# Performance work log

Hardware: AMD Instinct MI355X
Metric: run time of the kernel (lower is better)

Reference implementation:

```python
import jax, jax.numpy as jnp
import numpy as np

B, L, D, H, S = 4, 4096, 1024, 16, 4
DH = D // H


def setup_inputs() -> dict:
    key = jax.random.key(0)
    ks = jax.random.split(key, 12)
    std = 0.02
    inp = {
        "x": jax.random.normal(ks[0], (B, L, D), jnp.float32),
        "scale_logits": jax.random.normal(ks[1], (S,), jnp.float32),
        "wq": jax.random.normal(ks[2], (D, D), jnp.float32) * std,
        "bq": jnp.zeros((D,), jnp.float32),
        "wk": jax.random.normal(ks[3], (D, D), jnp.float32) * std,
        "bk": jnp.zeros((D,), jnp.float32),
        "wv": jax.random.normal(ks[4], (D, D), jnp.float32) * std,
        "bv": jnp.zeros((D,), jnp.float32),
        "wo": jax.random.normal(ks[5], (D, D), jnp.float32) * std,
        "bo": jnp.zeros((D,), jnp.float32),
        "ws": jax.random.normal(ks[6], (S, D, D), jnp.float32) * std,  # per-scale Linear weights (out,in)
        "bs": jax.random.normal(ks[7], (S, D), jnp.float32) * std,
    }
    return inp


def reference(x, scale_logits, wq, bq, wk, bk, wv, bv, wo, bo, ws, bs):
    # q/k/v projections; kept flat (B,L,D) since the torch code re-flattens before scale proj
    qf = x @ wq.T + bq
    kf = x @ wk.T + bk
    vf = x @ wv.T + bv
    # per-scale linear projection, vectorized over scales: (B,S,L,D)
    sq = jnp.einsum('bld,sed->bsle', qf, ws) + bs[None, :, None, :]
    sk = jnp.einsum('bld,sed->bsle', kf, ws) + bs[None, :, None, :]
    sv = jnp.einsum('bld,sed->bsle', vf, ws) + bs[None, :, None, :]
    sq = sq.reshape(B, S, L, H, DH)
    sk = sk.reshape(B, S, L, H, DH)
    sv = sv.reshape(B, S, L, H, DH)
    # faithful to torch: matmul over last two dims of (B,L,H,dh) -> per-position
    # head-mixing scores of shape (B,S,L,H,H)
    scale = 1.0 / np.sqrt(DH).astype(np.float32)
    scores = jnp.einsum('bslhd,bslgd->bslhg', sq, sk) * scale
    attn = jax.nn.softmax(scores, axis=-1)
    out = jnp.einsum('bslhg,bslgd->bslhd', attn, sv)  # (B,S,L,H,DH)
    w = jax.nn.softmax(scale_logits, axis=0)  # (S,)
    combined = jnp.einsum('s,bslhd->blhd', w, out).reshape(B, L, D)
    return combined @ wo.T + bo
```

## Files before the change

### kernel.cpp

```cpp
#include <hip/hip_runtime.h>


typedef unsigned short u16;
typedef __attribute__((ext_vector_type(8))) short s16x8;
typedef __attribute__((ext_vector_type(8))) unsigned short u16x8;
typedef __attribute__((ext_vector_type(4))) float f32x4;

#define MM 16384
#define DDIM 1024
#define DDSQ 1048576ull

__device__ __forceinline__ u16 f2bf(float f) {
  unsigned u = __float_as_uint(f);
  u = (u + 0x7FFFu + ((u >> 16) & 1u)) >> 16;
  return (u16)u;
}
__device__ __forceinline__ float b2f(u16 b) {
  return __uint_as_float(((unsigned)b) << 16);
}
__device__ __forceinline__ void gload_lds16(const void* g, void* l) {
  __builtin_amdgcn_global_load_lds(
      (const __attribute__((address_space(1))) void*)g,
      (__attribute__((address_space(3))) void*)l, 16, 0, 0);
}

__global__ __launch_bounds__(256) void k_f32_to_bf16(
    const float* __restrict__ in, u16* __restrict__ out, int n4) {
  int i = blockIdx.x * 256 + threadIdx.x;
  if (i >= n4) return;
  float4 v = reinterpret_cast<const float4*>(in)[i];
  ushort4 o;
  o.x = f2bf(v.x); o.y = f2bf(v.y); o.z = f2bf(v.z); o.w = f2bf(v.w);
  reinterpret_cast<ushort4*>(out)[i] = o;
}

__global__ __launch_bounds__(256) void k_transpose_bf16(
    const float* __restrict__ wq, const float* __restrict__ wk,
    const float* __restrict__ wv, u16* __restrict__ out) {
  __shared__ float tile[32][33];
  const float* src = (blockIdx.z == 0) ? wq : (blockIdx.z == 1) ? wk : wv;
  u16* dst = out + (size_t)blockIdx.z * DDSQ;
  int tx = threadIdx.x, ty = threadIdx.y;
  int bx = blockIdx.x * 32, by = blockIdx.y * 32;
#pragma unroll
  for (int i = 0; i < 4; ++i)
    tile[ty + 8 * i][tx] = src[(size_t)(by + ty + 8 * i) * DDIM + bx + tx];
  __syncthreads();
#pragma unroll
  for (int i = 0; i < 4; ++i)
    dst[(size_t)(bx + ty + 8 * i) * DDIM + by + tx] = f2bf(tile[tx][ty + 8 * i]);
}

__global__ __launch_bounds__(256) void k_bias_fuse(
    const float* __restrict__ ws, const float* __restrict__ bq,
    const float* __restrict__ bk, const float* __restrict__ bv,
    const float* __restrict__ bs, float* __restrict__ bf) {
  int idx = blockIdx.y;
  int s = idx / 3, t = idx - s * 3;
  const float* bt = (t == 0) ? bq : (t == 1) ? bk : bv;
  int lane = threadIdx.x & 63, wid = threadIdx.x >> 6;
  int e = blockIdx.x * 4 + wid;
  const float* wr = ws + (size_t)s * DDSQ + (size_t)e * DDIM;
  float p = 0.f;
  for (int j = lane; j < DDIM; j += 64) p += wr[j] * bt[j];
#pragma unroll
  for (int off = 32; off > 0; off >>= 1) p += __shfl_xor(p, off);
  if (lane == 0) bf[idx * DDIM + e] = p + bs[s * DDIM + e];
}

template <typename OutT>
__global__ __launch_bounds__(256) void k_gemm_bt(
    const u16* __restrict__ A, const u16* __restrict__ B, OutT* __restrict__ C,
    const float* __restrict__ bias, int M, int N, int K,
    size_t za, size_t zb, size_t zc, size_t zbias, int zmode) {
  __shared__ u16 lds_a[128 * 32];
  __shared__ u16 lds_b[128 * 32];

  int z = blockIdx.x >> 3;
  int n_blk = blockIdx.x & 7;
  int m_blk = blockIdx.y;
  if (zmode == 1) { A += (size_t)(z / 3) * za; B += (size_t)(z % 3) * zb; }
  else            { A += (size_t)z * za;       B += (size_t)z * zb; }
  C += (size_t)z * zc;
  const float* biasz = bias ? (bias + (size_t)z * zbias) : nullptr;

  int m0 = m_blk * 128, n0 = n_blk * 128;
  int tid = threadIdx.x;
  int lane = tid & 63, wid = tid >> 6;
  int wm = wid >> 1, wn = wid & 1;

  f32x4 acc[4][4] = {};

  auto stage = [&](int k0) {
#pragma unroll
    for (int i = 0; i < 2; ++i) {
      int c = wid * 2 + i;
      int row = c * 16 + (lane >> 2);
      int col = (lane & 3) * 8;
      gload_lds16(A + (size_t)(m0 + row) * K + k0 + col, &lds_a[c * 512]);
      gload_lds16(B + (size_t)(n0 + row) * K + k0 + col, &lds_b[c * 512]);
    }
  };

  stage(0);
  int ar = (wm * 64 + (lane & 15)) * 32 + (lane >> 4) * 8;
  int br = (wn * 64 + (lane & 15)) * 32 + (lane >> 4) * 8;
  for (int k0 = 0;;) {
    __syncthreads();
    s16x8 af[4], bfr[4];
#pragma unroll
    for (int mi = 0; mi < 4; ++mi)
      af[mi] = *reinterpret_cast<const s16x8*>(&lds_a[ar + mi * 16 * 32]);
#pragma unroll
    for (int ni = 0; ni < 4; ++ni)
      bfr[ni] = *reinterpret_cast<const s16x8*>(&lds_b[br + ni * 16 * 32]);
#pragma unroll
    for (int mi = 0; mi < 4; ++mi)
#pragma unroll
      for (int ni = 0; ni < 4; ++ni)
        acc[mi][ni] = __builtin_amdgcn_mfma_f32_16x16x32_bf16(
            af[mi], bfr[ni], acc[mi][ni], 0, 0, 0);
    k0 += 32;
    if (k0 >= K) break;
    __syncthreads();
    stage(k0);
  }

#pragma unroll
  for (int mi = 0; mi < 4; ++mi) {
#pragma unroll
    for (int ni = 0; ni < 4; ++ni) {
      int colg = n0 + wn * 64 + ni * 16 + (lane & 15);
      float badd = biasz ? biasz[colg] : 0.f;
#pragma unroll
      for (int r = 0; r < 4; ++r) {
        int rowg = m0 + wm * 64 + mi * 16 + ((lane >> 4) << 2) + r;
        float v = acc[mi][ni][r] + badd;
        if constexpr (sizeof(OutT) == 2) C[(size_t)rowg * N + colg] = f2bf(v);
        else                             C[(size_t)rowg * N + colg] = v;
      }
    }
  }
}

template <typename OutT>
__global__ __launch_bounds__(512, 1) void k_gemm256(
    const u16* __restrict__ A, const u16* __restrict__ B, OutT* __restrict__ C,
    const float* __restrict__ bias, int M, int N, int K,
    size_t za, size_t zb, size_t zc, size_t zbias, int nbx) {
  __shared__ u16 lds[4][2][8192];

  int z = blockIdx.x / nbx;
  int nb = blockIdx.x - z * nbx;
  const u16* Ag = A + (size_t)z * za;
  const u16* Bg = B + (size_t)z * zb;
  OutT* Cg = C + (size_t)z * zc;
  const float* biasz = bias + (size_t)z * zbias;

  int m0 = blockIdx.y * 256, n0 = nb * 256;
  int tid = threadIdx.x;
  int lane = tid & 63, wid = tid >> 6;
  int wm = wid >> 2, wn = wid & 3;
  int NT = K >> 5;

  int scb = ((lane & 3) * 16) ^ (((lane >> 3) & 3) << 4);
  const char* srcA[2]; const char* srcB[2]; int ldsc[2];
#pragma unroll
  for (int r = 0; r < 2; ++r) {
    int c = r * 8 + wid;
    int row = c * 16 + (lane >> 2);
    srcA[r] = (const char*)Ag + ((size_t)(m0 + row) * K) * 2 + scb;
    srcB[r] = (const char*)Bg + ((size_t)(n0 + row) * K) * 2 + scb;
    ldsc[r] = c * 1024;
  }
  char* lbase = (char*)&lds[0][0][0];

  int fxor = ((lane >> 4) * 16) ^ (((lane >> 1) & 3) << 4);
  int aoff = (wm * 128 + (lane & 15)) * 64 + fxor;
  int boff = (wn * 64 + (lane & 15)) * 64 + fxor;

  f32x4 acc[8][4] = {};

#define STAGE_A(kt, rg)                                                   \
  {                                                                       \
    _Pragma("unroll") for (int r = 0; r < 2; ++r)                         \
        gload_lds16(srcA[r] + (size_t)(kt) * 64,                          \
                    lbase + (rg) * 32768 + ldsc[r]);                      \
  }
#define STAGE_B(kt, rg)                                                   \
  {                                                                       \
    _Pragma("unroll") for (int r = 0; r < 2; ++r)                         \
        gload_lds16(srcB[r] + (size_t)(kt) * 64,                          \
                    lbase + (rg) * 32768 + 16384 + ldsc[r]);              \
  }

  STAGE_A(0, 0); STAGE_B(0, 0);
  STAGE_A(1, 1); STAGE_B(1, 1);
  STAGE_A(2, 2); STAGE_B(2, 2);
  asm volatile("s_waitcnt vmcnt(8)" ::: "memory");
  asm volatile("s_barrier" ::: "memory");

  for (int t = 0; t < NT; ++t) {
    int rg = t & 3;
    int t3 = (t + 3 < NT) ? t + 3 : NT - 1;
    int rg3 = (rg + 3) & 3;
    const char* bA = lbase + rg * 32768;
    const char* bB = bA + 16384;

    s16x8 fb[4], fa[4], fa2[4];
#pragma unroll
    for (int ni = 0; ni < 4; ++ni)
      fb[ni] = *(const s16x8*)(bB + boff + ni * 1024);
#pragma unroll
    for (int mi = 0; mi < 4; ++mi)
      fa[mi] = *(const s16x8*)(bA + aoff + mi * 1024);
    STAGE_A(t3, rg3);
#pragma unroll
    for (int mi = 0; mi < 4; ++mi)
      fa2[mi] = *(const s16x8*)(bA + aoff + 4096 + mi * 1024);
    STAGE_B(t3, rg3);

    __builtin_amdgcn_s_setprio(1);
#pragma unroll
    for (int mi = 0; mi < 4; ++mi)
#pragma unroll
      for (int ni = 0; ni < 4; ++ni)
        acc[mi][ni] = __builtin_amdgcn_mfma_f32_16x16x32_bf16(
            fa[mi], fb[ni], acc[mi][ni], 0, 0, 0);
#pragma unroll
    for (int mi = 0; mi < 4; ++mi)
#pragma unroll
      for (int ni = 0; ni < 4; ++ni)
        acc[mi + 4][ni] = __builtin_amdgcn_mfma_f32_16x16x32_bf16(
            fa2[mi], fb[ni], acc[mi + 4][ni], 0, 0, 0);
    __builtin_amdgcn_s_setprio(0);

    asm volatile("s_waitcnt vmcnt(8)" ::: "memory");
    asm volatile("s_barrier" ::: "memory");
  }
#undef STAGE_A
#undef STAGE_B

  asm volatile("s_waitcnt vmcnt(0)" ::: "memory");

#pragma unroll
  for (int mi = 0; mi < 8; ++mi) {
#pragma unroll
    for (int ni = 0; ni < 4; ++ni) {
      int colg = n0 + wn * 64 + ni * 16 + (lane & 15);
      float badd = biasz[colg];
#pragma unroll
      for (int r = 0; r < 4; ++r) {
        int rowg = m0 + wm * 128 + mi * 16 + ((lane >> 4) << 2) + r;
        float v = acc[mi][ni][r] + badd;
        if constexpr (sizeof(OutT) == 2) Cg[(size_t)rowg * N + colg] = f2bf(v);
        else                             Cg[(size_t)rowg * N + colg] = v;
      }
    }
  }
}

__global__ __launch_bounds__(256) void k_attn_all(
    const u16* __restrict__ proj, u16* __restrict__ outbf,
    const float* __restrict__ sl, int rows) {
  __shared__ u16 kv[4][2][1024];
  int lane = threadIdx.x & 63, wid = threadIdx.x >> 6;
  int row = blockIdx.x * 4 + wid;
  int h = lane >> 2, dq = lane & 3;
  int doff = h * 64 + dq * 16;

  float l0 = sl[0], l1 = sl[1], l2 = sl[2], l3 = sl[3];
  float lm = fmaxf(fmaxf(l0, l1), fmaxf(l2, l3));
  float e0 = __expf(l0 - lm), e1 = __expf(l1 - lm), e2 = __expf(l2 - lm),
        e3 = __expf(l3 - lm);
  float esum = e0 + e1 + e2 + e3;
  float wsc4[4] = {e0 / esum, e1 / esum, e2 / esum, e3 / esum};

  float acc[16];
#pragma unroll
  for (int i = 0; i < 16; ++i) acc[i] = 0.f;

  for (int s = 0; s < 4; ++s) {
    const u16* kr = proj + ((size_t)(3 * s + 1) * rows + row) * DDIM;
    const u16* vr = proj + ((size_t)(3 * s + 2) * rows + row) * DDIM;
    asm volatile("s_waitcnt vmcnt(0) lgkmcnt(0)" ::: "memory");
    gload_lds16(kr + lane * 8,       &kv[wid][0][0]);
    gload_lds16(kr + 512 + lane * 8, &kv[wid][0][512]);
    gload_lds16(vr + lane * 8,       &kv[wid][1][0]);
    gload_lds16(vr + 512 + lane * 8, &kv[wid][1][512]);

    const u16* qr = proj + ((size_t)(3 * s) * rows + row) * DDIM + doff;
    u16x8 q0 = *reinterpret_cast<const u16x8*>(qr);
    u16x8 q1 = *reinterpret_cast<const u16x8*>(qr + 8);
    float qf[16];
#pragma unroll
    for (int i = 0; i < 8; ++i) {
      qf[i]     = b2f(q0[i]) * 0.125f;
      qf[8 + i] = b2f(q1[i]) * 0.125f;
    }
    asm volatile("s_waitcnt vmcnt(0)" ::: "memory");

    float sc[16];
#pragma unroll
    for (int g = 0; g < 16; ++g) {
      const u16* kp = &kv[wid][0][g * 64 + dq * 16];
      u16x8 k0 = *reinterpret_cast<const u16x8*>(kp);
      u16x8 k1 = *reinterpret_cast<const u16x8*>(kp + 8);
      float d = 0.f;
#pragma unroll
      for (int i = 0; i < 8; ++i) d = fmaf(qf[i], b2f(k0[i]), d);
#pragma unroll
      for (int i = 0; i < 8; ++i) d = fmaf(qf[8 + i], b2f(k1[i]), d);
      d += __shfl_xor(d, 1);
      d += __shfl_xor(d, 2);
      sc[g] = d;
    }

    float mx = sc[0];
#pragma unroll
    for (int g = 1; g < 16; ++g) mx = fmaxf(mx, sc[g]);
    float sum = 0.f;
#pragma unroll
    for (int g = 0; g < 16; ++g) { sc[g] = __expf(sc[g] - mx); sum += sc[g]; }
    float inv = wsc4[s] / sum;
#pragma unroll
    for (int g = 0; g < 16; ++g) sc[g] *= inv;

#pragma unroll
    for (int g = 0; g < 16; ++g) {
      float a = sc[g];
      const u16* vp = &kv[wid][1][g * 64 + dq * 16];
      u16x8 v0 = *reinterpret_cast<const u16x8*>(vp);
      u16x8 v1 = *reinterpret_cast<const u16x8*>(vp + 8);
#pragma unroll
      for (int i = 0; i < 8; ++i) {
        acc[i]     = fmaf(a, b2f(v0[i]), acc[i]);
        acc[8 + i] = fmaf(a, b2f(v1[i]), acc[8 + i]);
      }
    }
  }

  u16* op = outbf + (size_t)row * DDIM + doff;
  u16x8 o0, o1;
#pragma unroll
  for (int i = 0; i < 8; ++i) {
    o0[i] = f2bf(acc[i]);
    o1[i] = f2bf(acc[8 + i]);
  }
  *reinterpret_cast<u16x8*>(op) = o0;
  *reinterpret_cast<u16x8*>(op + 8) = o1;
}

extern "C" void kernel_launch(void* const* d_in, const int* in_sizes, int n_in,
                              void* d_out, int out_size, void* d_ws,
                              size_t ws_size, hipStream_t stream) {
  const float* x  = (const float*)d_in[0];
  const float* sl = (const float*)d_in[1];
  const float* wq = (const float*)d_in[2];
  const float* bq = (const float*)d_in[3];
  const float* wk = (const float*)d_in[4];
  const float* bk = (const float*)d_in[5];
  const float* wv = (const float*)d_in[6];
  const float* bv = (const float*)d_in[7];
  const float* wo = (const float*)d_in[8];
  const float* bo = (const float*)d_in[9];
  const float* ws = (const float*)d_in[10];
  const float* bs = (const float*)d_in[11];
  float* out = (float*)d_out;

  char* wsb = (char*)d_ws;
  size_t off = 0;
  u16* xbf    = (u16*)(wsb + off); off += (size_t)MM * DDIM * 2;
  u16* wfus   = (u16*)(wsb + off); off += 12ull * DDSQ * 2;
  u16* wobf   = (u16*)(wsb + off); off += DDSQ * 2;
  float* bfus = (float*)(wsb + off); off += 65536;
  u16* combc  = (u16*)(wsb + off); off += (size_t)MM * DDIM * 2;
  char* dynr  = wsb + off;
  size_t fixed = off;

  int chunk = 4096;
  while (chunk > 1024 && fixed + (size_t)12 * chunk * DDIM * 2 > ws_size)
    chunk >>= 1;
  u16* projc = (u16*)dynr;
  u16* wtT  = (u16*)dynr;
  u16* wsbf = (u16*)(dynr + 3ull * DDSQ * 2);

  int n4;
  n4 = MM * DDIM / 4;
  k_f32_to_bf16<<<(n4 + 255) / 256, 256, 0, stream>>>(x, xbf, n4);
  n4 = (int)(4 * DDSQ / 4);
  k_f32_to_bf16<<<(n4 + 255) / 256, 256, 0, stream>>>(ws, wsbf, n4);
  n4 = (int)(DDSQ / 4);
  k_f32_to_bf16<<<(n4 + 255) / 256, 256, 0, stream>>>(wo, wobf, n4);

  k_transpose_bf16<<<dim3(32, 32, 3), dim3(32, 8), 0, stream>>>(wq, wk, wv, wtT);
  k_bias_fuse<<<dim3(256, 12), 256, 0, stream>>>(ws, bq, bk, bv, bs, bfus);

  k_gemm_bt<u16><<<dim3(96, 8), 256, 0, stream>>>(
      wsbf, wtT, wfus, nullptr, 1024, 1024, 1024, DDSQ, DDSQ, DDSQ, 0, 1);

  int nchunks = MM / chunk;
  for (int c = 0; c < nchunks; ++c) {
    const u16* xa = xbf + (size_t)c * chunk * DDIM;
    k_gemm256<u16><<<dim3(48, chunk / 256), 512, 0, stream>>>(
        xa, wfus, projc, bfus, chunk, 1024, 1024,
        0, DDSQ, (size_t)chunk * DDIM, DDIM, 4);
    k_attn_all<<<dim3(chunk / 4), 256, 0, stream>>>(
        projc, combc + (size_t)c * chunk * DDIM, sl, chunk);
  }

  k_gemm256<float><<<dim3(4, 64), 512, 0, stream>>>(
      combc, wobf, out, bo, MM, 1024, 1024, 0, 0, 0, 0, 4);
}
```

Baseline: 723.4 us.

## Double-buffer LDS fragments in GEMM and prefetch K/V stages in attention

In the GEMM main loop, the LDS-to-register fragment loads for the next k-tile are issued before the current tile's MFMAs, using ping-pong register sets over a loop unrolled by two. The aim is to hide LDS read latency behind the matrix ops. The attention kernel now loads all four scales' Q up front and double-buffers K/V in LDS, prefetching two scales ahead so global loads overlap the compute for the current scale. This costs more registers and twice the attention LDS, and the hand-written vmcnt waits assume an exact count of outstanding loads, which could create races if that count is wrong.

```diff
diff --git a/kernel.cpp b/kernel.cpp
--- a/kernel.cpp
+++ b/kernel.cpp
@@ -180,6 +180,8 @@
   int boff = (wn * 64 + (lane & 15)) * 64 + fxor;
 
   f32x4 acc[8][4] = {};
+  s16x8 cA0[4], cA1[4], cB[4];
+  s16x8 nA0[4], nA1[4], nB[4];
 
 #define STAGE_A(kt, rg)                                                   \
   {                                                                       \
@@ -194,50 +196,56 @@
                     lbase + (rg) * 32768 + 16384 + ldsc[r]);              \
   }
 
+#define SUBITER(C0, C1, CBv, N0, N1, NBv, tcur)                           \
+  {                                                                       \
+    asm volatile("s_waitcnt vmcnt(4)" ::: "memory");                      \
+    asm volatile("s_barrier" ::: "memory");                               \
+    int tn = (tcur) + 1 < NT ? (tcur) + 1 : NT - 1;                       \
+    const char* bA = lbase + (tn & 3) * 32768;                            \
+    const char* bB = bA + 16384;                                          \
+    _Pragma("unroll") for (int i = 0; i < 4; ++i)                         \
+        NBv[i] = *(const s16x8*)(bB + boff + i * 1024);                   \
+    _Pragma("unroll") for (int i = 0; i < 4; ++i)                         \
+        N0[i] = *(const s16x8*)(bA + aoff + i * 1024);                    \
+    _Pragma("unroll") for (int i = 0; i < 4; ++i)                         \
+        N1[i] = *(const s16x8*)(bA + aoff + 4096 + i * 1024);             \
+    int ts = (tcur) + 3 < NT ? (tcur) + 3 : NT - 1;                       \
+    int rgs = ((tcur) + 3) & 3;                                           \
+    STAGE_A(ts, rgs); STAGE_B(ts, rgs);                                   \
+    __builtin_amdgcn_s_setprio(1);                                        \
+    _Pragma("unroll") for (int mi = 0; mi < 4; ++mi)                      \
+      _Pragma("unroll") for (int ni = 0; ni < 4; ++ni)                    \
+          acc[mi][ni] = __builtin_amdgcn_mfma_f32_16x16x32_bf16(          \
+              C0[mi], CBv[ni], acc[mi][ni], 0, 0, 0);                     \
+    _Pragma("unroll") for (int mi = 0; mi < 4; ++mi)                      \
+      _Pragma("unroll") for (int ni = 0; ni < 4; ++ni)                    \
+          acc[mi + 4][ni] = __builtin_amdgcn_mfma_f32_16x16x32_bf16(      \
+              C1[mi], CBv[ni], acc[mi + 4][ni], 0, 0, 0);                 \
+    __builtin_amdgcn_s_setprio(0);                                        \
+  }
+
   STAGE_A(0, 0); STAGE_B(0, 0);
   STAGE_A(1, 1); STAGE_B(1, 1);
   STAGE_A(2, 2); STAGE_B(2, 2);
   asm volatile("s_waitcnt vmcnt(8)" ::: "memory");
   asm volatile("s_barrier" ::: "memory");
-
-  for (int t = 0; t < NT; ++t) {
-    int rg = t & 3;
-    int t3 = (t + 3 < NT) ? t + 3 : NT - 1;
-    int rg3 = (rg + 3) & 3;
-    const char* bA = lbase + rg * 32768;
+  {
+    const char* bA = lbase;
     const char* bB = bA + 16384;
-
-    s16x8 fb[4], fa[4], fa2[4];
-#pragma unroll
-    for (int ni = 0; ni < 4; ++ni)
-      fb[ni] = *(const s16x8*)(bB + boff + ni * 1024);
-#pragma unroll
-    for (int mi = 0; mi < 4; ++mi)
-      fa[mi] = *(const s16x8*)(bA + aoff + mi * 1024);
-    STAGE_A(t3, rg3);
-#pragma unroll
-    for (int mi = 0; mi < 4; ++mi)
-      fa2[mi] = *(const s16x8*)(bA + aoff + 4096 + mi * 1024);
-    STAGE_B(t3, rg3);
-
-    __builtin_amdgcn_s_setprio(1);
-#pragma unroll
-    for (int mi = 0; mi < 4; ++mi)
-#pragma unroll
-      for (int ni = 0; ni < 4; ++ni)
-        acc[mi][ni] = __builtin_amdgcn_mfma_f32_16x16x32_bf16(
-            fa[mi], fb[ni], acc[mi][ni], 0, 0, 0);
-#pragma unroll
-    for (int mi = 0; mi < 4; ++mi)
-#pragma unroll
-      for (int ni = 0; ni < 4; ++ni)
-        acc[mi + 4][ni] = __builtin_amdgcn_mfma_f32_16x16x32_bf16(
-            fa2[mi], fb[ni], acc[mi + 4][ni], 0, 0, 0);
-    __builtin_amdgcn_s_setprio(0);
-
-    asm volatile("s_waitcnt vmcnt(8)" ::: "memory");
-    asm volatile("s_barrier" ::: "memory");
-  }
+#pragma unroll
+    for (int i = 0; i < 4; ++i) cB[i]  = *(const s16x8*)(bB + boff + i * 1024);
+#pragma unroll
+    for (int i = 0; i < 4; ++i) cA0[i] = *(const s16x8*)(bA + aoff + i * 1024);
+#pragma unroll
+    for (int i = 0; i < 4; ++i)
+      cA1[i] = *(const s16x8*)(bA + aoff + 4096 + i * 1024);
+  }
+
+  for (int t = 0; t < NT; t += 2) {
+    SUBITER(cA0, cA1, cB, nA0, nA1, nB, t);
+    SUBITER(nA0, nA1, nB, cA0, cA1, cB, t + 1);
+  }
+#undef SUBITER
 #undef STAGE_A
 #undef STAGE_B
 
@@ -263,7 +271,7 @@
 __global__ __launch_bounds__(256) void k_attn_all(
     const u16* __restrict__ proj, u16* __restrict__ outbf,
     const float* __restrict__ sl, int rows) {
-  __shared__ u16 kv[4][2][1024];
+  __shared__ u16 kv[4][2][2][1024];
   int lane = threadIdx.x & 63, wid = threadIdx.x >> 6;
   int row = blockIdx.x * 4 + wid;
   int h = lane >> 2, dq = lane & 3;
@@ -276,34 +284,48 @@
   float esum = e0 + e1 + e2 + e3;
   float wsc4[4] = {e0 / esum, e1 / esum, e2 / esum, e3 / esum};
 
+  u16x8 q0[4], q1[4];
+#pragma unroll
+  for (int s = 0; s < 4; ++s) {
+    const u16* qr = proj + ((size_t)(3 * s) * rows + row) * DDIM + doff;
+    q0[s] = *reinterpret_cast<const u16x8*>(qr);
+    q1[s] = *reinterpret_cast<const u16x8*>(qr + 8);
+  }
+  asm volatile("" ::: "memory");
+
+#define KV_ISSUE(s, buf)                                                   \
+  {                                                                        \
+    const u16* kr = proj + ((size_t)(3 * (s) + 1) * rows + row) * DDIM;    \
+    const u16* vr = proj + ((size_t)(3 * (s) + 2) * rows + row) * DDIM;    \
+    gload_lds16(kr + lane * 8,       &kv[wid][buf][0][0]);                 \
+    gload_lds16(kr + 512 + lane * 8, &kv[wid][buf][0][512]);               \
+    gload_lds16(vr + lane * 8,       &kv[wid][buf][1][0]);                 \
+    gload_lds16(vr + 512 + lane * 8, &kv[wid][buf][1][512]);               \
+  }
+
+  KV_ISSUE(0, 0);
+  KV_ISSUE(1, 1);
+
   float acc[16];
 #pragma unroll
   for (int i = 0; i < 16; ++i) acc[i] = 0.f;
 
+#pragma unroll
   for (int s = 0; s < 4; ++s) {
-    const u16* kr = proj + ((size_t)(3 * s + 1) * rows + row) * DDIM;
-    const u16* vr = proj + ((size_t)(3 * s + 2) * rows + row) * DDIM;
-    asm volatile("s_waitcnt vmcnt(0) lgkmcnt(0)" ::: "memory");
-    gload_lds16(kr + lane * 8,       &kv[wid][0][0]);
-    gload_lds16(kr + 512 + lane * 8, &kv[wid][0][512]);
-    gload_lds16(vr + lane * 8,       &kv[wid][1][0]);
-    gload_lds16(vr + 512 + lane * 8, &kv[wid][1][512]);
-
-    const u16* qr = proj + ((size_t)(3 * s) * rows + row) * DDIM + doff;
-    u16x8 q0 = *reinterpret_cast<const u16x8*>(qr);
-    u16x8 q1 = *reinterpret_cast<const u16x8*>(qr + 8);
+    if (s < 3) asm volatile("s_waitcnt vmcnt(4)" ::: "memory");
+    else       asm volatile("s_waitcnt vmcnt(0)" ::: "memory");
+
     float qf[16];
 #pragma unroll
     for (int i = 0; i < 8; ++i) {
-      qf[i]     = b2f(q0[i]) * 0.125f;
-      qf[8 + i] = b2f(q1[i]) * 0.125f;
-    }
-    asm volatile("s_waitcnt vmcnt(0)" ::: "memory");
+      qf[i]     = b2f(q0[s][i]) * 0.125f;
+      qf[8 + i] = b2f(q1[s][i]) * 0.125f;
+    }
 
     float sc[16];
 #pragma unroll
     for (int g = 0; g < 16; ++g) {
-      const u16* kp = &kv[wid][0][g * 64 + dq * 16];
+      const u16* kp = &kv[wid][s & 1][0][g * 64 + dq * 16];
       u16x8 k0 = *reinterpret_cast<const u16x8*>(kp);
       u16x8 k1 = *reinterpret_cast<const u16x8*>(kp + 8);
       float d = 0.f;
@@ -329,7 +351,7 @@
 #pragma unroll
     for (int g = 0; g < 16; ++g) {
       float a = sc[g];
-      const u16* vp = &kv[wid][1][g * 64 + dq * 16];
+      const u16* vp = &kv[wid][s & 1][1][g * 64 + dq * 16];
       u16x8 v0 = *reinterpret_cast<const u16x8*>(vp);
       u16x8 v1 = *reinterpret_cast<const u16x8*>(vp + 8);
 #pragma unroll
@@ -338,7 +360,14 @@
         acc[8 + i] = fmaf(a, b2f(v1[i]), acc[8 + i]);
       }
     }
-  }
+
+    if (s < 2) {
+      asm volatile("s_waitcnt lgkmcnt(0)" ::: "memory");
+      __builtin_amdgcn_sched_barrier(0);
+      KV_ISSUE(s + 2, s & 1);
+    }
+  }
+#undef KV_ISSUE
 
   u16* op = outbf + (size_t)row * DDIM + doff;
   u16x8 o0, o1;
```

Measured after the change: 1.038 ms. 43.5% more time.
